# Kernel optimization log

Hardware: AMD Instinct MI355X
Metric: run time of the kernel (lower is better)

The kernel has to match this reference:

```python
import jax, jax.numpy as jnp
import numpy as np

N, IN_DIM, H_DIM, POS_DIM, K, M, E, OUT_DIM = 50000, 256, 96, 32, 64, 128, 800000, 40
HID = H_DIM + POS_DIM  # 128

def _lin(key, fan_out, fan_in):
    k1, k2 = jax.random.split(key)
    bnd = 1.0 / np.sqrt(fan_in)
    W = jax.random.uniform(k1, (fan_out, fan_in), minval=-bnd, maxval=bnd, dtype=jnp.float32)
    b = jax.random.uniform(k2, (fan_out,), minval=-bnd, maxval=bnd, dtype=jnp.float32)
    return W, b

def setup_inputs() -> dict:
    key = jax.random.key(0)
    ks = jax.random.split(key, 12)
    x = jax.random.normal(ks[0], (N, IN_DIM), dtype=jnp.float32)
    eigenvectors = jax.random.normal(ks[1], (N, M), dtype=jnp.float32)
    eigenvalues = jax.random.uniform(ks[2], (M,), dtype=jnp.float32)
    edge_index = jax.random.randint(ks[3], (2, E), 0, N, dtype=jnp.int64)
    W_feat, b_feat = _lin(ks[4], H_DIM, IN_DIM)
    alpha = jax.random.uniform(ks[5], (K, POS_DIM), minval=-1/np.sqrt(K), maxval=1/np.sqrt(K), dtype=jnp.float32)
    Wl1, bl1 = _lin(ks[6], HID, HID)
    Wr1, _ = _lin(ks[7], HID, HID)
    Wl2, bl2 = _lin(ks[8], HID, HID)
    Wr2, _ = _lin(ks[9], HID, HID)
    W_ro, b_ro = _lin(ks[10], OUT_DIM, HID)
    return dict(x=x, eigenvectors=eigenvectors, eigenvalues=eigenvalues, edge_index=edge_index,
                W_feat=W_feat, b_feat=b_feat, alpha=alpha,
                Wl1=Wl1, bl1=bl1, Wr1=Wr1, Wl2=Wl2, bl2=bl2, Wr2=Wr2,
                W_ro=W_ro, b_ro=b_ro)

def _sage_conv(x, src, dst, Wl, bl, Wr):
    # PyG SAGEConv (mean aggr): out = lin_l(mean_{j->i} x_j) + lin_r(x_i)
    n = x.shape[0]
    agg = jax.ops.segment_sum(x[src], dst, num_segments=n)           # [N, HID]
    cnt = jax.ops.segment_sum(jnp.ones_like(dst, dtype=x.dtype), dst, num_segments=n)
    mean = agg / jnp.maximum(cnt, 1.0)[:, None]
    return mean @ Wl.T + bl + x @ Wr.T

def reference(x, eigenvectors, eigenvalues, edge_index,
              W_feat, b_feat, alpha, Wl1, bl1, Wr1, Wl2, bl2, Wr2, W_ro, b_ro):
    # normalize eigenvectors per column to [-1, 1]
    ev_min = jnp.min(eigenvectors, axis=0, keepdims=True)
    ev_max = jnp.max(eigenvectors, axis=0, keepdims=True)
    ev = (eigenvectors - ev_min) / (ev_max - ev_min) * 2.0 - 1.0
    # normalize eigenvalues to [-1, 1], Chebyshev basis via arccos/cos
    lmin, lmax = jnp.min(eigenvalues), jnp.max(eigenvalues)
    lam = (eigenvalues - lmin) / (lmax - lmin) * 2.0 - 1.0
    theta = jnp.arccos(lam)[:, None] * jnp.arange(K, dtype=lam.dtype)[None, :]  # [M, K]
    pe = jnp.cos(theta) @ alpha                                                  # [M, pos_dim]
    pos = ev @ pe                                                                # [N, pos_dim]
    h = jnp.concatenate([x @ W_feat.T + b_feat, pos], axis=-1)                   # [N, HID]
    src, dst = edge_index[0], edge_index[1]
    h = jax.nn.relu(_sage_conv(h, src, dst, Wl1, bl1, Wr1))
    h = jax.nn.relu(_sage_conv(h, src, dst, Wl2, bl2, Wr2))
    out = jax.nn.log_softmax(h @ W_ro.T + b_ro, axis=-1)
    return out, pe
```

## Files before the change

kernel.cpp:

```cpp
#include <hip/hip_runtime.h>
#include <math.h>

#define N        50000
#define IN_DIM   256
#define H_DIM    96
#define POS_DIM  32
#define KCH      64
#define M        128
#define NE       800000
#define OUT_DIM  40
#define HID      128
#define NSCAN    196
#define NTILES   ((N + 63) / 64)
#define NBK      391
#define BKCAP    2560
#define NSCATB   512
#define SREG     1563

typedef __attribute__((ext_vector_type(8))) short short8v;
typedef __attribute__((ext_vector_type(4))) float float4v;

__device__ __forceinline__ unsigned short f2bf(float f){
  unsigned u = __float_as_uint(f);
  u += 0x7fffu + ((u >> 16) & 1u);
  return (unsigned short)(u >> 16);
}
__device__ __forceinline__ float bf_lo(unsigned u){ return __uint_as_float(u << 16); }
__device__ __forceinline__ float bf_hi(unsigned u){ return __uint_as_float(u & 0xffff0000u); }

__device__ __forceinline__ unsigned enc_key(float f){
  unsigned u = __float_as_uint(f);
  return (u & 0x80000000u) ? ~u : (u | 0x80000000u);
}
__device__ __forceinline__ float dec_key(unsigned k){
  unsigned u = (k & 0x80000000u) ? (k ^ 0x80000000u) : ~k;
  return __uint_as_float(u);
}

__global__ void k_init(unsigned* __restrict__ encmn, unsigned* __restrict__ encmx,
                       short* __restrict__ WT_pos, int* __restrict__ bkt_cnt){
  int i = blockIdx.x*blockDim.x + threadIdx.x;
  if (i < M){ encmn[i] = 0xFFFFFFFFu; encmx[i] = 0u; }
  if (i < M*M) WT_pos[i] = 0;
  if (i < NBK) bkt_cnt[i] = 0;
}

__global__ __launch_bounds__(256) void k_f1(const float* __restrict__ ev,
    unsigned* __restrict__ encmn, unsigned* __restrict__ encmx,
    const int* __restrict__ dst, int* __restrict__ bkt_cnt){
  int tid = threadIdx.x;
  if (blockIdx.x < 256){
    __shared__ float4 smn[256], smx[256];
    int cg  = tid & 31;
    int rs  = blockIdx.x*8 + (tid >> 5);
    float4 mn = make_float4( 3.4e38f,  3.4e38f,  3.4e38f,  3.4e38f);
    float4 mx = make_float4(-3.4e38f, -3.4e38f, -3.4e38f, -3.4e38f);
    #pragma unroll 4
    for (int r = rs; r < N; r += 2048){
      float4 v = *(const float4*)&ev[(size_t)r*M + cg*4];
      mn.x = fminf(mn.x, v.x); mn.y = fminf(mn.y, v.y);
      mn.z = fminf(mn.z, v.z); mn.w = fminf(mn.w, v.w);
      mx.x = fmaxf(mx.x, v.x); mx.y = fmaxf(mx.y, v.y);
      mx.z = fmaxf(mx.z, v.z); mx.w = fmaxf(mx.w, v.w);
    }
    smn[tid] = mn; smx[tid] = mx;
    __syncthreads();
    for (int s = 128; s >= 32; s >>= 1){
      if (tid < s){
        float4 a = smn[tid], b = smn[tid + s];
        smn[tid] = make_float4(fminf(a.x,b.x), fminf(a.y,b.y), fminf(a.z,b.z), fminf(a.w,b.w));
        float4 c = smx[tid], d = smx[tid + s];
        smx[tid] = make_float4(fmaxf(c.x,d.x), fmaxf(c.y,d.y), fmaxf(c.z,d.z), fmaxf(c.w,d.w));
      }
      __syncthreads();
    }
    if (tid < 32){
      float4 a = smn[tid], b = smx[tid];
      atomicMin(&encmn[tid*4+0], enc_key(a.x));
      atomicMin(&encmn[tid*4+1], enc_key(a.y));
      atomicMin(&encmn[tid*4+2], enc_key(a.z));
      atomicMin(&encmn[tid*4+3], enc_key(a.w));
      atomicMax(&encmx[tid*4+0], enc_key(b.x));
      atomicMax(&encmx[tid*4+1], enc_key(b.y));
      atomicMax(&encmx[tid*4+2], enc_key(b.z));
      atomicMax(&encmx[tid*4+3], enc_key(b.w));
    }
  } else {
    __shared__ int hh[NBK];
    int bid = blockIdx.x - 256;
    for (int i = tid; i < NBK; i += 256) hh[i] = 0;
    __syncthreads();
    for (int e = bid*256 + tid; e < NE; e += 512*256)
      atomicAdd(&hh[dst[e] >> 7], 1);
    __syncthreads();
    for (int i = tid; i < NBK; i += 256){
      int c = hh[i];
      if (c) atomicAdd(&bkt_cnt[i], c);
    }
  }
}

__global__ __launch_bounds__(512) void k_f2(
    const float* __restrict__ eigval, const float* __restrict__ alpha,
    const unsigned* __restrict__ encmn, const unsigned* __restrict__ encmx,
    const float* __restrict__ Wf, const float* __restrict__ bfeat,
    const float* __restrict__ Wl1, const float* __restrict__ Wr1,
    const float* __restrict__ Wl2, const float* __restrict__ Wr2,
    const float* __restrict__ Wro, const float* __restrict__ bro,
    short* __restrict__ WT_pos, float* __restrict__ pe_raw, float* __restrict__ pe_out,
    short* __restrict__ WTf, float* __restrict__ biasf,
    short* __restrict__ Wc1, short* __restrict__ Wc2,
    short* __restrict__ WTro, float* __restrict__ biasro,
    const int* __restrict__ bkt_cnt, int* __restrict__ bkt_start,
    int* __restrict__ bkt_cursor){
  int tid = threadIdx.x;
  if (blockIdx.x < 8){
    __shared__ float rmn[128], rmx[128];
    if (tid < 128){ float v = eigval[tid]; rmn[tid] = v; rmx[tid] = v; }
    __syncthreads();
    for (int s = 64; s; s >>= 1){
      if (tid < s){ rmn[tid] = fminf(rmn[tid], rmn[tid+s]); rmx[tid] = fmaxf(rmx[tid], rmx[tid+s]); }
      __syncthreads();
    }
    float lmin = rmn[0], lmax = rmx[0];
    int g = blockIdx.x*512 + tid;
    int m = g >> 5, p = g & 31;
    float v = eigval[m];
    float lam = (v - lmin)/(lmax - lmin)*2.0f - 1.0f;
    lam = fminf(1.0f, fmaxf(-1.0f, lam));
    float t0 = 1.0f, t1 = lam;
    float acc = alpha[p] + lam*alpha[POS_DIM + p];
    float two_lam = lam + lam;
    #pragma unroll
    for (int k = 2; k < KCH; ++k){
      float t2 = fmaf(two_lam, t1, -t0);
      acc = fmaf(t2, alpha[k*POS_DIM + p], acc);
      t0 = t1; t1 = t2;
    }
    pe_out[g] = acc;
    pe_raw[g] = acc;
    float cmn = dec_key(encmn[m]);
    float cmx = dec_key(encmx[m]);
    float A = 2.0f/(cmx - cmn);
    WT_pos[p*M + m] = (short)f2bf(A*acc);
    for (int i = g; i < 128*256; i += 4096){
      int c = i >> 8, k = i & 255;
      WTf[i] = (c < H_DIM) ? (short)f2bf(Wf[c*IN_DIM + k]) : (short)0;
      Wc1[i] = (short)f2bf((k < HID) ? Wl1[c*HID + k] : Wr1[c*HID + k - HID]);
      Wc2[i] = (short)f2bf((k < HID) ? Wl2[c*HID + k] : Wr2[c*HID + k - HID]);
    }
    for (int i = g; i < 48*128; i += 4096){
      int c = i >> 7, k = i & 127;
      WTro[i] = (c < OUT_DIM) ? (short)f2bf(Wro[c*HID + k]) : (short)0;
    }
    if (g < 128) biasf[g] = (g < H_DIM) ? bfeat[g] : 0.f;
    if (g >= 128 && g < 176) biasro[g - 128] = (g - 128 < OUT_DIM) ? bro[g - 128] : 0.f;
  } else {
    __shared__ int s[512];
    int t = tid;
    int v = (t < NBK) ? bkt_cnt[t] : 0;
    s[t] = v;
    __syncthreads();
    for (int st = 1; st < 512; st <<= 1){
      int a = (t >= st) ? s[t-st] : 0;
      __syncthreads();
      s[t] += a;
      __syncthreads();
    }
    int excl = s[t] - v;
    if (t < NBK){ bkt_start[t] = excl; bkt_cursor[t] = excl; }
    if (t == 0) bkt_start[NBK] = NE;
  }
}

__global__ __launch_bounds__(256) void k_f3(const int* __restrict__ src,
    const int* __restrict__ dst, int* __restrict__ bkt_cursor,
    unsigned* __restrict__ estage,
    const unsigned* __restrict__ encmn, const unsigned* __restrict__ encmx,
    const float* __restrict__ pe_raw, float* __restrict__ bias_pos){
  int tid = threadIdx.x;
  if (blockIdx.x < NSCATB){
    __shared__ int lcnt[NBK];
    __shared__ int lbase[NBK];
    int e0 = blockIdx.x*SREG;
    int e1 = min(e0 + SREG, NE);
    for (int i = tid; i < NBK; i += 256) lcnt[i] = 0;
    __syncthreads();
    for (int e = e0 + tid; e < e1; e += 256)
      atomicAdd(&lcnt[dst[e] >> 7], 1);
    __syncthreads();
    for (int i = tid; i < NBK; i += 256){
      int c = lcnt[i];
      lbase[i] = c ? atomicAdd(&bkt_cursor[i], c) : 0;
      lcnt[i] = 0;
    }
    __syncthreads();
    for (int e = e0 + tid; e < e1; e += 256){
      int d = dst[e];
      int b = d >> 7;
      int slot = lbase[b] + atomicAdd(&lcnt[b], 1);
      estage[slot] = (unsigned)src[e] | ((unsigned)(d & 127) << 16);
    }
  } else {
    __shared__ float s[256];
    int p = tid >> 3, c = tid & 7;
    float sum = 0.f;
    for (int m = c*16; m < c*16 + 16; ++m){
      float cmn = dec_key(encmn[m]);
      float cmx = dec_key(encmx[m]);
      float A = 2.0f/(cmx - cmn);
      float B = -cmn*A - 1.0f;
      sum += B*pe_raw[m*POS_DIM + p];
    }
    s[tid] = sum;
    __syncthreads();
    if (c == 0){
      float t = 0.f;
      #pragma unroll
      for (int j = 0; j < 8; ++j) t += s[p*8 + j];
      bias_pos[p] = t;
    }
  }
}

__global__ __launch_bounds__(256) void k_f4(
    const int* __restrict__ bkt_start, const unsigned* __restrict__ estage,
    unsigned short* __restrict__ csr, int* __restrict__ row_ptr,
    const float* __restrict__ x, const float* __restrict__ ev,
    const short* __restrict__ WTf, const float* __restrict__ biasf,
    const short* __restrict__ WT_pos, const float* __restrict__ bias_pos,
    unsigned short* __restrict__ outp)
{
  __shared__ __align__(16) char smem[64*384*2];
  int tid = threadIdx.x;
  if (blockIdx.x < NBK){
    unsigned* eb = (unsigned*)smem;
    int* ncnt = (int*)(smem + BKCAP*4);
    int* sc   = ncnt + 128;
    int* noff = sc + 128;
    int b = blockIdx.x;
    int s = bkt_start[b], e = bkt_start[b+1];
    int cnt = min(e - s, BKCAP);
    for (int i = tid; i < cnt; i += 256) eb[i] = estage[s + i];
    if (tid < 128) ncnt[tid] = 0;
    __syncthreads();
    for (int i = tid; i < cnt; i += 256)
      atomicAdd(&ncnt[(eb[i] >> 16) & 127], 1);
    __syncthreads();
    if (tid < 128) sc[tid] = ncnt[tid];
    __syncthreads();
    for (int st = 1; st < 128; st <<= 1){
      int a = (tid < 128 && tid >= st) ? sc[tid-st] : 0;
      __syncthreads();
      if (tid < 128) sc[tid] += a;
      __syncthreads();
    }
    if (tid < 128){
      int excl = sc[tid] - ncnt[tid];
      noff[tid] = excl;
      int node = b*128 + tid;
      if (node <= N) row_ptr[node] = s + excl;
      ncnt[tid] = 0;
    }
    __syncthreads();
    for (int i = tid; i < cnt; i += 256){
      unsigned v = eb[i];
      int ld = (v >> 16) & 127;
      int slot = noff[ld] + atomicAdd(&ncnt[ld], 1);
      csr[s + slot] = (unsigned short)(v & 0xffffu);
    }
    return;
  }
  short* a_lds = (short*)smem;
  int wid = tid >> 6, lane = tid & 63;
  int lrow = lane & 15, lk = (lane >> 4)*8;
  bool isPos = (wid == 3);

  short8v bfragF[8][2];
  short8v bfragP[4][2];
  float b0, b1;
  if (!isPos){
    int colBase = wid*32;
    #pragma unroll
    for (int s = 0; s < 8; ++s)
      #pragma unroll
      for (int ct = 0; ct < 2; ++ct){
        int col = colBase + ct*16 + lrow;
        bfragF[s][ct] = *(const short8v*)&WTf[col*256 + s*32 + lk];
      }
    b0 = biasf[colBase + lrow]; b1 = biasf[colBase + 16 + lrow];
  } else {
    #pragma unroll
    for (int s = 0; s < 4; ++s)
      #pragma unroll
      for (int ct = 0; ct < 2; ++ct){
        int col = ct*16 + lrow;
        bfragP[s][ct] = *(const short8v*)&WT_pos[col*128 + s*32 + lk];
      }
    b0 = bias_pos[lrow]; b1 = bias_pos[16 + lrow];
  }

  for (int tile = blockIdx.x - NBK; tile < NTILES; tile += gridDim.x - NBK){
    int n0 = tile*64;
    __syncthreads();
    for (int c = tid; c < 64*48; c += 256){
      int row = c / 48, k8 = c % 48;
      int gn = min(n0 + row, N-1);
      const float* src = (k8 < 32) ? &x[(size_t)gn*IN_DIM + k8*8]
                                   : &ev[(size_t)gn*M + (k8-32)*8];
      float4v f0 = *(const float4v*)src;
      float4v f1 = *(const float4v*)(src + 4);
      short8v vv;
      vv[0] = (short)f2bf(f0[0]); vv[1] = (short)f2bf(f0[1]);
      vv[2] = (short)f2bf(f0[2]); vv[3] = (short)f2bf(f0[3]);
      vv[4] = (short)f2bf(f1[0]); vv[5] = (short)f2bf(f1[1]);
      vv[6] = (short)f2bf(f1[2]); vv[7] = (short)f2bf(f1[3]);
      unsigned off = (unsigned)(row*768 + k8*16) ^ (unsigned)((row & 7) << 4);
      *(short8v*)((char*)a_lds + off) = vv;
    }
    __syncthreads();
    float4v acc[4][2];
    #pragma unroll
    for (int nt = 0; nt < 4; ++nt){
      acc[nt][0] = (float4v){0.f,0.f,0.f,0.f};
      acc[nt][1] = (float4v){0.f,0.f,0.f,0.f};
    }
    if (!isPos){
      #pragma unroll
      for (int s = 0; s < 8; ++s)
        #pragma unroll
        for (int nt = 0; nt < 4; ++nt){
          int row = nt*16 + lrow;
          unsigned off = (unsigned)(row*768 + (s*32 + lk)*2) ^ (unsigned)((row & 7) << 4);
          short8v a = *(const short8v*)((const char*)a_lds + off);
          acc[nt][0] = __builtin_amdgcn_mfma_f32_16x16x32_bf16(a, bfragF[s][0], acc[nt][0], 0, 0, 0);
          acc[nt][1] = __builtin_amdgcn_mfma_f32_16x16x32_bf16(a, bfragF[s][1], acc[nt][1], 0, 0, 0);
        }
    } else {
      #pragma unroll
      for (int s = 0; s < 4; ++s)
        #pragma unroll
        for (int nt = 0; nt < 4; ++nt){
          int row = nt*16 + lrow;
          unsigned off = (unsigned)(row*768 + 512 + (s*32 + lk)*2) ^ (unsigned)((row & 7) << 4);
          short8v a = *(const short8v*)((const char*)a_lds + off);
          acc[nt][0] = __builtin_amdgcn_mfma_f32_16x16x32_bf16(a, bfragP[s][0], acc[nt][0], 0, 0, 0);
          acc[nt][1] = __builtin_amdgcn_mfma_f32_16x16x32_bf16(a, bfragP[s][1], acc[nt][1], 0, 0, 0);
        }
    }
    int colBase = isPos ? 96 : wid*32;
    int rbase = (lane >> 4)*4;
    #pragma unroll
    for (int nt = 0; nt < 4; ++nt)
      #pragma unroll
      for (int ct = 0; ct < 2; ++ct){
        int col = colBase + ct*16 + lrow;
        float bb = ct ? b1 : b0;
        #pragma unroll
        for (int r = 0; r < 4; ++r){
          int node = n0 + nt*16 + rbase + r;
          if (node < N) outp[(size_t)node*HID + col] = f2bf(acc[nt][ct][r] + bb);
        }
      }
  }
}

__global__ __launch_bounds__(256) void k_agg_b(const unsigned* __restrict__ h,
    const int* __restrict__ row_ptr, const unsigned short* __restrict__ csr,
    unsigned* __restrict__ outm){
  int gid = blockIdx.x*blockDim.x + threadIdx.x;
  int i = gid >> 6;
  int lane = gid & 63;
  if (i >= N) return;
  int grp = lane >> 4;
  int lc  = lane & 15;
  int b = row_ptr[i], e = row_ptr[i+1];
  float a0[8] = {0,0,0,0,0,0,0,0}, a1[8] = {0,0,0,0,0,0,0,0};
  float a2[8] = {0,0,0,0,0,0,0,0}, a3[8] = {0,0,0,0,0,0,0,0};
  int j = b + grp;
  for (; j + 12 < e; j += 16){
    uint4 v0 = *(const uint4*)&h[(size_t)csr[j]*64    + lc*4];
    uint4 v1 = *(const uint4*)&h[(size_t)csr[j+4]*64  + lc*4];
    uint4 v2 = *(const uint4*)&h[(size_t)csr[j+8]*64  + lc*4];
    uint4 v3 = *(const uint4*)&h[(size_t)csr[j+12]*64 + lc*4];
    a0[0] += bf_lo(v0.x); a0[1] += bf_hi(v0.x); a0[2] += bf_lo(v0.y); a0[3] += bf_hi(v0.y);
    a0[4] += bf_lo(v0.z); a0[5] += bf_hi(v0.z); a0[6] += bf_lo(v0.w); a0[7] += bf_hi(v0.w);
    a1[0] += bf_lo(v1.x); a1[1] += bf_hi(v1.x); a1[2] += bf_lo(v1.y); a1[3] += bf_hi(v1.y);
    a1[4] += bf_lo(v1.z); a1[5] += bf_hi(v1.z); a1[6] += bf_lo(v1.w); a1[7] += bf_hi(v1.w);
    a2[0] += bf_lo(v2.x); a2[1] += bf_hi(v2.x); a2[2] += bf_lo(v2.y); a2[3] += bf_hi(v2.y);
    a2[4] += bf_lo(v2.z); a2[5] += bf_hi(v2.z); a2[6] += bf_lo(v2.w); a2[7] += bf_hi(v2.w);
    a3[0] += bf_lo(v3.x); a3[1] += bf_hi(v3.x); a3[2] += bf_lo(v3.y); a3[3] += bf_hi(v3.y);
    a3[4] += bf_lo(v3.z); a3[5] += bf_hi(v3.z); a3[6] += bf_lo(v3.w); a3[7] += bf_hi(v3.w);
  }
  for (; j < e; j += 4){
    uint4 v0 = *(const uint4*)&h[(size_t)csr[j]*64 + lc*4];
    a0[0] += bf_lo(v0.x); a0[1] += bf_hi(v0.x); a0[2] += bf_lo(v0.y); a0[3] += bf_hi(v0.y);
    a0[4] += bf_lo(v0.z); a0[5] += bf_hi(v0.z); a0[6] += bf_lo(v0.w); a0[7] += bf_hi(v0.w);
  }
  #pragma unroll
  for (int k = 0; k < 8; ++k){
    float t = (a0[k] + a1[k]) + (a2[k] + a3[k]);
    t += __shfl_xor(t, 16, 64);
    t += __shfl_xor(t, 32, 64);
    a0[k] = t;
  }
  if (grp == 0){
    float inv = 1.0f / fmaxf((float)(e - b), 1.0f);
    uint4 o;
    o.x = (unsigned)f2bf(a0[0]*inv) | ((unsigned)f2bf(a0[1]*inv) << 16);
    o.y = (unsigned)f2bf(a0[2]*inv) | ((unsigned)f2bf(a0[3]*inv) << 16);
    o.z = (unsigned)f2bf(a0[4]*inv) | ((unsigned)f2bf(a0[5]*inv) << 16);
    o.w = (unsigned)f2bf(a0[6]*inv) | ((unsigned)f2bf(a0[7]*inv) << 16);
    *(uint4*)&outm[(size_t)i*64 + lc*4] = o;
  }
}

__global__ __launch_bounds__(256) void k_conv(
    const short* __restrict__ A0, const short* __restrict__ A1,
    const short* __restrict__ WT, const float* __restrict__ bias,
    unsigned short* __restrict__ outp)
{
  __shared__ short a_lds[64*256];
  int tid = threadIdx.x;
  int wid = tid >> 6, lane = tid & 63;
  int colBase = wid*32;
  int lrow = lane & 15, lk = (lane >> 4)*8;

  short8v bfrag[8][2];
  #pragma unroll
  for (int s = 0; s < 8; ++s)
    #pragma unroll
    for (int ct = 0; ct < 2; ++ct){
      int col = colBase + ct*16 + lrow;
      bfrag[s][ct] = *(const short8v*)&WT[col*256 + s*32 + lk];
    }
  float b0 = bias[colBase + lrow], b1 = bias[colBase + 16 + lrow];

  for (int tile = blockIdx.x; tile < NTILES; tile += gridDim.x){
    int n0 = tile*64;
    __syncthreads();
    #pragma unroll
    for (int c = tid; c < 64*32; c += 256){
      int row = c >> 5, k8 = c & 31;
      int gn = min(n0 + row, N-1);
      const short* src = (k8 < 16) ? (A0 + (size_t)gn*HID + k8*8)
                                   : (A1 + (size_t)gn*HID + (k8-16)*8);
      short8v vv = *(const short8v*)src;
      unsigned off = (unsigned)(row*512 + k8*16) ^ (unsigned)((row & 7) << 4);
      *(short8v*)((char*)a_lds + off) = vv;
    }
    __syncthreads();
    float4v acc[4][2];
    #pragma unroll
    for (int nt = 0; nt < 4; ++nt){
      acc[nt][0] = (float4v){0.f,0.f,0.f,0.f};
      acc[nt][1] = (float4v){0.f,0.f,0.f,0.f};
    }
    #pragma unroll
    for (int s = 0; s < 8; ++s)
      #pragma unroll
      for (int nt = 0; nt < 4; ++nt){
        int row = nt*16 + lrow;
        unsigned off = (unsigned)(row*512 + (s*32 + lk)*2) ^ (unsigned)((row & 7) << 4);
        short8v a = *(const short8v*)((const char*)a_lds + off);
        acc[nt][0] = __builtin_amdgcn_mfma_f32_16x16x32_bf16(a, bfrag[s][0], acc[nt][0], 0, 0, 0);
        acc[nt][1] = __builtin_amdgcn_mfma_f32_16x16x32_bf16(a, bfrag[s][1], acc[nt][1], 0, 0, 0);
      }
    int rbase = (lane >> 4)*4;
    #pragma unroll
    for (int nt = 0; nt < 4; ++nt)
      #pragma unroll
      for (int ct = 0; ct < 2; ++ct){
        int col = colBase + ct*16 + lrow;
        float bb = ct ? b1 : b0;
        #pragma unroll
        for (int r = 0; r < 4; ++r){
          int node = n0 + nt*16 + rbase + r;
          if (node < N)
            outp[(size_t)node*HID + col] = f2bf(fmaxf(acc[nt][ct][r] + bb, 0.f));
        }
      }
  }
}

__global__ __launch_bounds__(256) void k_conv_ro(
    const short* __restrict__ A0, const short* __restrict__ A1,
    const short* __restrict__ WT, const float* __restrict__ bias,
    const short* __restrict__ WTro, const float* __restrict__ biasro,
    float* __restrict__ out)
{
  __shared__ short a_lds[64*256];
  __shared__ short o_lds[64*128];
  int tid = threadIdx.x;
  int wid = tid >> 6, lane = tid & 63;
  int colBase = wid*32;
  int lrow = lane & 15, lk = (lane >> 4)*8;

  short8v bfrag[8][2];
  #pragma unroll
  for (int s = 0; s < 8; ++s)
    #pragma unroll
    for (int ct = 0; ct < 2; ++ct){
      int col = colBase + ct*16 + lrow;
      bfrag[s][ct] = *(const short8v*)&WT[col*256 + s*32 + lk];
    }
  float b0 = bias[colBase + lrow], b1 = bias[colBase + 16 + lrow];

  short8v bfragR[4][3];
  #pragma unroll
  for (int s = 0; s < 4; ++s)
    #pragma unroll
    for (int t = 0; t < 3; ++t){
      int col = t*16 + lrow;
      bfragR[s][t] = *(const short8v*)&WTro[col*HID + s*32 + lk];
    }
  float biasR[3] = { biasro[lrow], biasro[16 + lrow], biasro[32 + lrow] };
  bool val2 = lrow < 8;

  for (int tile = blockIdx.x; tile < NTILES; tile += gridDim.x){
    int n0 = tile*64;
    __syncthreads();
    #pragma unroll
    for (int c = tid; c < 64*32; c += 256){
      int row = c >> 5, k8 = c & 31;
      int gn = min(n0 + row, N-1);
      const short* src = (k8 < 16) ? (A0 + (size_t)gn*HID + k8*8)
                                   : (A1 + (size_t)gn*HID + (k8-16)*8);
      short8v vv = *(const short8v*)src;
      unsigned off = (unsigned)(row*512 + k8*16) ^ (unsigned)((row & 7) << 4);
      *(short8v*)((char*)a_lds + off) = vv;
    }
    __syncthreads();
    float4v acc[4][2];
    #pragma unroll
    for (int nt = 0; nt < 4; ++nt){
      acc[nt][0] = (float4v){0.f,0.f,0.f,0.f};
      acc[nt][1] = (float4v){0.f,0.f,0.f,0.f};
    }
    #pragma unroll
    for (int s = 0; s < 8; ++s)
      #pragma unroll
      for (int nt = 0; nt < 4; ++nt){
        int row = nt*16 + lrow;
        unsigned off = (unsigned)(row*512 + (s*32 + lk)*2) ^ (unsigned)((row & 7) << 4);
        short8v a = *(const short8v*)((const char*)a_lds + off);
        acc[nt][0] = __builtin_amdgcn_mfma_f32_16x16x32_bf16(a, bfrag[s][0], acc[nt][0], 0, 0, 0);
        acc[nt][1] = __builtin_amdgcn_mfma_f32_16x16x32_bf16(a, bfrag[s][1], acc[nt][1], 0, 0, 0);
      }
    int rbase = (lane >> 4)*4;
    #pragma unroll
    for (int nt = 0; nt < 4; ++nt)
      #pragma unroll
      for (int ct = 0; ct < 2; ++ct){
        int col = colBase + ct*16 + lrow;
        float bb = ct ? b1 : b0;
        #pragma unroll
        for (int r = 0; r < 4; ++r){
          int row = nt*16 + rbase + r;
          float v = fmaxf(acc[nt][ct][r] + bb, 0.f);
          unsigned off = (unsigned)(row*256 + col*2) ^ (unsigned)((row & 7) << 4);
          *(short*)((char*)o_lds + off) = (short)f2bf(v);
        }
      }
    __syncthreads();
    float4v acc3[3];
    acc3[0] = (float4v){0.f,0.f,0.f,0.f};
    acc3[1] = (float4v){0.f,0.f,0.f,0.f};
    acc3[2] = (float4v){0.f,0.f,0.f,0.f};
    #pragma unroll
    for (int s = 0; s < 4; ++s){
      int row = wid*16 + lrow;
      unsigned off = (unsigned)(row*256 + (s*32 + lk)*2) ^ (unsigned)((row & 7) << 4);
      short8v a = *(const short8v*)((const char*)o_lds + off);
      acc3[0] = __builtin_amdgcn_mfma_f32_16x16x32_bf16(a, bfragR[s][0], acc3[0], 0, 0, 0);
      acc3[1] = __builtin_amdgcn_mfma_f32_16x16x32_bf16(a, bfragR[s][1], acc3[1], 0, 0, 0);
      acc3[2] = __builtin_amdgcn_mfma_f32_16x16x32_bf16(a, bfragR[s][2], acc3[2], 0, 0, 0);
    }
    #pragma unroll
    for (int r = 0; r < 4; ++r){
      float v0 = acc3[0][r] + biasR[0];
      float v1 = acc3[1][r] + biasR[1];
      float v2 = acc3[2][r] + biasR[2];
      float mx = fmaxf(v0, v1);
      mx = fmaxf(mx, val2 ? v2 : -3.4e38f);
      #pragma unroll
      for (int off = 1; off < 16; off <<= 1) mx = fmaxf(mx, __shfl_xor(mx, off, 64));
      float e = expf(v0 - mx) + expf(v1 - mx) + (val2 ? expf(v2 - mx) : 0.f);
      #pragma unroll
      for (int off = 1; off < 16; off <<= 1) e += __shfl_xor(e, off, 64);
      float lz = mx + logf(e);
      int node = n0 + wid*16 + (lane >> 4)*4 + r;
      if (node < N){
        out[(size_t)node*OUT_DIM + lrow]      = v0 - lz;
        out[(size_t)node*OUT_DIM + 16 + lrow] = v1 - lz;
        if (val2) out[(size_t)node*OUT_DIM + 32 + lrow] = v2 - lz;
      }
    }
  }
}

extern "C" void kernel_launch(void* const* d_in, const int* in_sizes, int n_in,
                              void* d_out, int out_size, void* d_ws, size_t ws_size,
                              hipStream_t stream){
  const float* x     = (const float*)d_in[0];
  const float* ev    = (const float*)d_in[1];
  const float* eigv  = (const float*)d_in[2];
  const int*   ei    = (const int*)d_in[3];
  const float* Wf    = (const float*)d_in[4];
  const float* bf    = (const float*)d_in[5];
  const float* alpha = (const float*)d_in[6];
  const float* Wl1   = (const float*)d_in[7];
  const float* bl1   = (const float*)d_in[8];
  const float* Wr1   = (const float*)d_in[9];
  const float* Wl2   = (const float*)d_in[10];
  const float* bl2   = (const float*)d_in[11];
  const float* Wr2   = (const float*)d_in[12];
  const float* Wro   = (const float*)d_in[13];
  const float* bro   = (const float*)d_in[14];
  float* out = (float*)d_out;

  short* h0b    = (short*)d_ws;
  short* h1b    = h0b + (size_t)N*HID;
  short* meanb  = h1b + (size_t)N*HID;
  short* WTf    = meanb + (size_t)N*HID;
  short* Wc1    = WTf + 128*256;
  short* Wc2    = Wc1 + 128*256;
  short* WT_pos = Wc2 + 128*256;
  short* WTro   = WT_pos + 128*128;
  float* biasf    = (float*)(WTro + 48*128);
  float* bias_pos = biasf + 128;
  float* biasro   = bias_pos + 128;
  unsigned* encmn = (unsigned*)(biasro + 48);
  unsigned* encmx = encmn + M;
  int* bkt_cnt    = (int*)(encmx + M);
  int* bkt_start  = bkt_cnt + NBK;
  int* bkt_cursor = bkt_start + NBK + 1;
  int* row_ptr    = bkt_cursor + NBK;
  unsigned* estage = (unsigned*)(row_ptr + N + 1);
  unsigned short* csr = (unsigned short*)(estage + NE);
  float* pe_raw = (float*)(csr + NE);

  const int* srcA = ei;
  const int* dstA = ei + NE;

  k_init<<<NSCAN, 256, 0, stream>>>(encmn, encmx, WT_pos, bkt_cnt);
  k_f1<<<768, 256, 0, stream>>>(ev, encmn, encmx, dstA, bkt_cnt);
  k_f2<<<9, 512, 0, stream>>>(eigv, alpha, encmn, encmx,
                              Wf, bf, Wl1, Wr1, Wl2, Wr2, Wro, bro,
                              WT_pos, pe_raw, out + (size_t)N*OUT_DIM,
                              WTf, biasf, Wc1, Wc2, WTro, biasro,
                              bkt_cnt, bkt_start, bkt_cursor);
  k_f3<<<NSCATB + 1, 256, 0, stream>>>(srcA, dstA, bkt_cursor, estage,
                                       encmn, encmx, pe_raw, bias_pos);
  k_f4<<<NBK + NTILES, 256, 0, stream>>>(bkt_start, estage, csr, row_ptr,
                                         x, ev, WTf, biasf, WT_pos, bias_pos,
                                         (unsigned short*)h0b);
  k_agg_b<<<(N*64)/256, 256, 0, stream>>>((const unsigned*)h0b, row_ptr, csr, (unsigned*)meanb);
  k_conv<<<NTILES, 256, 0, stream>>>(meanb, h0b, Wc1, bl1, (unsigned short*)h1b);
  k_agg_b<<<(N*64)/256, 256, 0, stream>>>((const unsigned*)h1b, row_ptr, csr, (unsigned*)meanb);
  k_conv_ro<<<NTILES, 256, 0, stream>>>(meanb, h1b, Wc2, bl2, WTro, biasro, out);
}
```

Before: 210.9 us.

## Split neighbor aggregation into four column passes to shrink per-pass gather footprint

The mean-aggregation kernel now launches four passes over the nodes. Each pass gathers only a 16-unsigned (32 bf16) column slice of every neighbor row with 4-byte loads instead of the full 128-wide row with 16-byte loads. The goal is a smaller working set of gathered data per pass so it fits in L2/MALL, cutting DRAM traffic from random neighbor reads. In exchange, csr and row_ptr are read four times, each gather moves only a 4-byte word per lane (partial cache-line use), and four times as many blocks are launched.

```diff
diff --git a/kernel.cpp b/kernel.cpp
--- a/kernel.cpp
+++ b/kernel.cpp
@@ -16,6 +16,7 @@
 #define BKCAP    2560
 #define NSCATB   512
 #define SREG     1563
+#define AGG_BPP  12500
 
 typedef __attribute__((ext_vector_type(8))) short short8v;
 typedef __attribute__((ext_vector_type(4))) float float4v;
@@ -368,50 +369,36 @@
 __global__ __launch_bounds__(256) void k_agg_b(const unsigned* __restrict__ h,
     const int* __restrict__ row_ptr, const unsigned short* __restrict__ csr,
     unsigned* __restrict__ outm){
-  int gid = blockIdx.x*blockDim.x + threadIdx.x;
-  int i = gid >> 6;
-  int lane = gid & 63;
-  if (i >= N) return;
+  int pass = blockIdx.x / AGG_BPP;
+  int node = (blockIdx.x % AGG_BPP)*4 + (threadIdx.x >> 6);
+  int lane = threadIdx.x & 63;
   int grp = lane >> 4;
-  int lc  = lane & 15;
-  int b = row_ptr[i], e = row_ptr[i+1];
-  float a0[8] = {0,0,0,0,0,0,0,0}, a1[8] = {0,0,0,0,0,0,0,0};
-  float a2[8] = {0,0,0,0,0,0,0,0}, a3[8] = {0,0,0,0,0,0,0,0};
+  int li  = lane & 15;
+  size_t coff = (size_t)pass*16 + li;
+  int b = row_ptr[node], e = row_ptr[node+1];
+  float s0=0.f,s1=0.f,t0=0.f,t1=0.f,u0=0.f,u1=0.f,v0=0.f,v1=0.f;
   int j = b + grp;
   for (; j + 12 < e; j += 16){
-    uint4 v0 = *(const uint4*)&h[(size_t)csr[j]*64    + lc*4];
-    uint4 v1 = *(const uint4*)&h[(size_t)csr[j+4]*64  + lc*4];
-    uint4 v2 = *(const uint4*)&h[(size_t)csr[j+8]*64  + lc*4];
-    uint4 v3 = *(const uint4*)&h[(size_t)csr[j+12]*64 + lc*4];
-    a0[0] += bf_lo(v0.x); a0[1] += bf_hi(v0.x); a0[2] += bf_lo(v0.y); a0[3] += bf_hi(v0.y);
-    a0[4] += bf_lo(v0.z); a0[5] += bf_hi(v0.z); a0[6] += bf_lo(v0.w); a0[7] += bf_hi(v0.w);
-    a1[0] += bf_lo(v1.x); a1[1] += bf_hi(v1.x); a1[2] += bf_lo(v1.y); a1[3] += bf_hi(v1.y);
-    a1[4] += bf_lo(v1.z); a1[5] += bf_hi(v1.z); a1[6] += bf_lo(v1.w); a1[7] += bf_hi(v1.w);
-    a2[0] += bf_lo(v2.x); a2[1] += bf_hi(v2.x); a2[2] += bf_lo(v2.y); a2[3] += bf_hi(v2.y);
-    a2[4] += bf_lo(v2.z); a2[5] += bf_hi(v2.z); a2[6] += bf_lo(v2.w); a2[7] += bf_hi(v2.w);
-    a3[0] += bf_lo(v3.x); a3[1] += bf_hi(v3.x); a3[2] += bf_lo(v3.y); a3[3] += bf_hi(v3.y);
-    a3[4] += bf_lo(v3.z); a3[5] += bf_hi(v3.z); a3[6] += bf_lo(v3.w); a3[7] += bf_hi(v3.w);
+    unsigned w0 = h[(size_t)csr[j]*64    + coff];
+    unsigned w1 = h[(size_t)csr[j+4]*64  + coff];
+    unsigned w2 = h[(size_t)csr[j+8]*64  + coff];
+    unsigned w3 = h[(size_t)csr[j+12]*64 + coff];
+    s0 += bf_lo(w0); s1 += bf_hi(w0);
+    t0 += bf_lo(w1); t1 += bf_hi(w1);
+    u0 += bf_lo(w2); u1 += bf_hi(w2);
+    v0 += bf_lo(w3); v1 += bf_hi(w3);
   }
   for (; j < e; j += 4){
-    uint4 v0 = *(const uint4*)&h[(size_t)csr[j]*64 + lc*4];
-    a0[0] += bf_lo(v0.x); a0[1] += bf_hi(v0.x); a0[2] += bf_lo(v0.y); a0[3] += bf_hi(v0.y);
-    a0[4] += bf_lo(v0.z); a0[5] += bf_hi(v0.z); a0[6] += bf_lo(v0.w); a0[7] += bf_hi(v0.w);
-  }
-  #pragma unroll
-  for (int k = 0; k < 8; ++k){
-    float t = (a0[k] + a1[k]) + (a2[k] + a3[k]);
-    t += __shfl_xor(t, 16, 64);
-    t += __shfl_xor(t, 32, 64);
-    a0[k] = t;
-  }
+    unsigned w0 = h[(size_t)csr[j]*64 + coff];
+    s0 += bf_lo(w0); s1 += bf_hi(w0);
+  }
+  float a0 = (s0 + t0) + (u0 + v0);
+  float a1 = (s1 + t1) + (u1 + v1);
+  a0 += __shfl_xor(a0, 16, 64); a0 += __shfl_xor(a0, 32, 64);
+  a1 += __shfl_xor(a1, 16, 64); a1 += __shfl_xor(a1, 32, 64);
   if (grp == 0){
     float inv = 1.0f / fmaxf((float)(e - b), 1.0f);
-    uint4 o;
-    o.x = (unsigned)f2bf(a0[0]*inv) | ((unsigned)f2bf(a0[1]*inv) << 16);
-    o.y = (unsigned)f2bf(a0[2]*inv) | ((unsigned)f2bf(a0[3]*inv) << 16);
-    o.z = (unsigned)f2bf(a0[4]*inv) | ((unsigned)f2bf(a0[5]*inv) << 16);
-    o.w = (unsigned)f2bf(a0[6]*inv) | ((unsigned)f2bf(a0[7]*inv) << 16);
-    *(uint4*)&outm[(size_t)i*64 + lc*4] = o;
+    outm[(size_t)node*64 + coff] = (unsigned)f2bf(a0*inv) | ((unsigned)f2bf(a1*inv) << 16);
   }
 }
 
@@ -655,8 +642,8 @@
   k_f4<<<NBK + NTILES, 256, 0, stream>>>(bkt_start, estage, csr, row_ptr,
                                          x, ev, WTf, biasf, WT_pos, bias_pos,
                                          (unsigned short*)h0b);
-  k_agg_b<<<(N*64)/256, 256, 0, stream>>>((const unsigned*)h0b, row_ptr, csr, (unsigned*)meanb);
+  k_agg_b<<<4*AGG_BPP, 256, 0, stream>>>((const unsigned*)h0b, row_ptr, csr, (unsigned*)meanb);
   k_conv<<<NTILES, 256, 0, stream>>>(meanb, h0b, Wc1, bl1, (unsigned short*)h1b);
-  k_agg_b<<<(N*64)/256, 256, 0, stream>>>((const unsigned*)h1b, row_ptr, csr, (unsigned*)meanb);
+  k_agg_b<<<4*AGG_BPP, 256, 0, stream>>>((const unsigned*)h1b, row_ptr, csr, (unsigned*)meanb);
   k_conv_ro<<<NTILES, 256, 0, stream>>>(meanb, h1b, Wc2, bl2, WTro, biasro, out);
 }
```

Measured after the change: 296.8 us. +40.8%, slower.
